# Kernel tuning notes

Hardware: AMD Instinct MI355X
Metric: run time of the kernel (lower is better)

## Reference

```python
import jax, jax.numpy as jnp
import numpy as np

B, L, H = 16, 4096, 256

def setup_inputs() -> dict:
    key = jax.random.key(0)
    k1, k2, k3 = jax.random.split(key, 3)
    scale = 1.0 / np.sqrt(H)
    x = jax.random.normal(k1, (B, L, H), dtype=jnp.float32)
    Wv = jax.random.normal(k2, (H, H), dtype=jnp.float32) * scale  # value_proj weight (torch Linear: y = x @ W.T)
    Wo = jax.random.normal(k3, (H, H), dtype=jnp.float32) * scale  # out_proj weight
    return {"x": x, "Wv": Wv, "Wo": Wo}

def reference(x, Wv, Wo):
    # x: [B, L, H]
    Bx, Lx, Hx = x.shape
    # Causal uniform-average 'attention' matrix: T[i, j] = 1/(i+1) for j <= i, else 0.
    tril = jnp.tril(jnp.ones((Lx, Lx), dtype=x.dtype))
    counts = jnp.arange(1, Lx + 1, dtype=x.dtype)[:, None]  # row-wise counts = i+1
    T = tril / counts
    # v = out_proj(value_proj(x)); torch Linear applies W.T on the right
    v = (x @ Wv.T) @ Wo.T                       # [B, L, H]
    # mixed[b, i] = mean over j <= i of v[b, j]  (== causal cumulative mean)
    mixed = jnp.einsum('ij,bjh->bih', T, v)     # [B, L, H]
    # dropout is identity in eval mode; pre_ln residual
    return x + mixed
```

## Files before the change

### kernel.cpp

```cpp
#include <hip/hip_runtime.h>
#include <hip/hip_bf16.h>


#define B_  16
#define L_  4096
#define H_  256
#define M_  (B_*L_)
#define CH  64
#define CHROWS 64
#define BM 64

typedef short short4v __attribute__((ext_vector_type(4)));
typedef short short8  __attribute__((ext_vector_type(8)));
typedef float f32x4   __attribute__((ext_vector_type(4)));

__device__ __forceinline__ unsigned short f2bf(float f) {
  unsigned int u = __builtin_bit_cast(unsigned int, f);
  u += 0x7fffu + ((u >> 16) & 1u);
  return (unsigned short)(u >> 16);
}
__device__ __forceinline__ float bf2f(unsigned short s) {
  return __builtin_bit_cast(float, ((unsigned int)s) << 16);
}

__global__ void fuse_w_kernel(const float* __restrict__ Wv,
                              const float* __restrict__ Wo,
                              unsigned short* __restrict__ Wbf) {
  __shared__ float wo[H_];
  int h = blockIdx.x, t = threadIdx.x;
  wo[t] = Wo[h*H_ + t];
  __syncthreads();
  float acc = 0.f;
  #pragma unroll 8
  for (int m = 0; m < H_; ++m) acc += wo[m] * Wv[m*H_ + t];
  Wbf[h*H_ + t] = f2bf(acc);
}

__global__ void partial_kernel(const float* __restrict__ x, float* __restrict__ P) {
  int c = blockIdx.x, b = blockIdx.y, t = threadIdx.x;
  const float* p = x + ((size_t)(b*L_ + c*CHROWS))*H_ + t;
  float s = 0.f;
  #pragma unroll 8
  for (int r = 0; r < CHROWS; ++r) s += p[(size_t)r*H_];
  P[(b*CH + c)*H_ + t] = s;
}

__global__ void scan_kernel(const float* __restrict__ P, float* __restrict__ O) {
  int b = blockIdx.x, t = threadIdx.x;
  float run = 0.f;
  #pragma unroll
  for (int c = 0; c < CH; ++c) {
    int idx = (b*CH + c)*H_ + t;
    O[idx] = run;
    run += P[idx];
  }
}

__global__ __launch_bounds__(512, 4) void main_kernel(
    const float* __restrict__ x,
    const unsigned short* __restrict__ Wbf,
    const float* __restrict__ Op,
    float* __restrict__ out) {
  __shared__ __align__(16) char smem[69632];
  float* zpart = (float*)(smem + 67584);

  const int tid = threadIdx.x;
  const int lane = tid & 63, wave = tid >> 6;
  const int rowBase = blockIdx.x * BM;

  float4 xk[8];
  const float* xb = x + (size_t)rowBase * H_;
  #pragma unroll
  for (int j = 0; j < 8; ++j)
    xk[j] = *(const float4*)(xb + (j*8 + wave)*H_ + lane*4);

  {
    const int c = tid & 255, h = tid >> 8;
    const float* op = Op + (size_t)blockIdx.x * H_ + h*128;
    const unsigned short* wr = Wbf + (size_t)c * H_ + h*128;
    float z = 0.f;
    #pragma unroll 4
    for (int kk = 0; kk < 16; ++kk) {
      short8 w8 = *(const short8*)(wr + kk*8);
      #pragma unroll
      for (int e = 0; e < 8; ++e) z += op[kk*8 + e] * bf2f((unsigned short)w8[e]);
    }
    zpart[h*256 + c] = z;
  }

  #pragma unroll
  for (int j = 0; j < 8; ++j) {
    int r = j*8 + wave;
    short4v s;
    s[0] = (short)f2bf(xk[j].x); s[1] = (short)f2bf(xk[j].y);
    s[2] = (short)f2bf(xk[j].z); s[3] = (short)f2bf(xk[j].w);
    *(short4v*)(smem + r*512 + ((lane*8) ^ ((r & 7) << 4))) = s;
  }
  __syncthreads();

  const int wc = wave;
  const int lrow = lane & 15, g = lane >> 4;
  f32x4 acc[4][2] = {};
  #pragma unroll
  for (int k0 = 0; k0 < 4; ++k0) {
    #pragma unroll
    for (int ks = 0; ks < 2; ++ks) {
      short8 bfr[2], af[4];
      #pragma unroll
      for (int n = 0; n < 2; ++n) {
        int wrow = wc*32 + n*16 + lrow;
        bfr[n] = *(const short8*)(Wbf + (size_t)wrow*H_ + k0*64 + ks*32 + g*8);
      }
      #pragma unroll
      for (int i = 0; i < 4; ++i) {
        int ar = i*16 + lrow;
        int cb = (k0*128 + ks*64 + g*16) ^ ((ar & 7) << 4);
        af[i] = *(const short8*)(smem + ar*512 + cb);
      }
      #pragma unroll
      for (int i = 0; i < 4; ++i)
        #pragma unroll
        for (int n = 0; n < 2; ++n)
          acc[i][n] = __builtin_amdgcn_mfma_f32_16x16x32_bf16(af[i], bfr[n], acc[i][n], 0, 0, 0);
    }
  }

  float base[2];
  #pragma unroll
  for (int n = 0; n < 2; ++n) {
    int c = wc*32 + n*16 + lrow;
    base[n] = zpart[c] + zpart[256 + c];
  }
  #pragma unroll
  for (int n = 0; n < 2; ++n) {
    float run = 0.f;
    #pragma unroll
    for (int i = 0; i < 4; ++i) {
      f32x4 a = acc[i][n];
      a[1] += a[0]; a[2] += a[1]; a[3] += a[2];
      float Bv = a[3];
      float v = Bv, t;
      t = __shfl_up(v, 16); if (lane >= 16) v += t;
      t = __shfl_up(v, 32); if (lane >= 32) v += t;
      float gex = v - Bv;
      float tot = __shfl(v, lrow + 48);
      float addv = gex + run + base[n];
      #pragma unroll
      for (int q = 0; q < 4; ++q) {
        int row = rowBase + i*16 + g*4 + q;
        float scale = 1.0f / (float)((row & (L_-1)) + 1);
        a[q] = (a[q] + addv) * scale;
      }
      acc[i][n] = a;
      run += tot;
    }
  }
  __syncthreads();

  #pragma unroll
  for (int i = 0; i < 4; ++i)
    #pragma unroll
    for (int n = 0; n < 2; ++n)
      #pragma unroll
      for (int q = 0; q < 4; ++q) {
        int row = i*16 + g*4 + q, col = wc*32 + n*16 + lrow;
        *(float*)(smem + row*1040 + col*4) = acc[i][n][q];
      }
  __syncthreads();

  float* ob = out + (size_t)rowBase * H_;
  #pragma unroll
  for (int j = 0; j < 8; ++j) {
    int r = j*8 + wave;
    f32x4 y = *(const f32x4*)(smem + r*1040 + lane*16);
    float4 o;
    o.x = xk[j].x + y[0]; o.y = xk[j].y + y[1];
    o.z = xk[j].z + y[2]; o.w = xk[j].w + y[3];
    *(float4*)(ob + r*H_ + lane*4) = o;
  }
}

extern "C" void kernel_launch(void* const* d_in, const int* in_sizes, int n_in,
                              void* d_out, int out_size, void* d_ws, size_t ws_size,
                              hipStream_t stream) {
  const float* x  = (const float*)d_in[0];
  const float* Wv = (const float*)d_in[1];
  const float* Wo = (const float*)d_in[2];
  float* out = (float*)d_out;

  char* ws = (char*)d_ws;
  unsigned short* Wbf = (unsigned short*)ws;
  float* P  = (float*)(ws + 131072);
  float* Op = (float*)(ws + 131072 + 1048576);

  hipLaunchKernelGGL(fuse_w_kernel,  dim3(H_),     dim3(H_), 0, stream, Wv, Wo, Wbf);
  hipLaunchKernelGGL(partial_kernel, dim3(CH, B_), dim3(H_), 0, stream, x, P);
  hipLaunchKernelGGL(scan_kernel,    dim3(B_),     dim3(H_), 0, stream, P, Op);
  hipLaunchKernelGGL(main_kernel,    dim3(M_/BM),  dim3(512), 0, stream,
                     x, Wbf, Op, out);
}
```

Before: 81.35 us.

## Halve main kernel block to 256 threads and stage output as bf16 in LDS

The main kernel now runs 4 waves per block instead of 8, and each wave computes 64 output columns (4x4 MFMA tiles) rather than 32. The carry-in vector z is computed by one thread per column without a split reduction. Output staging in shared memory switches from fp32 to swizzled bf16, shrinking LDS use so more blocks can be resident. Instead of keeping x in registers, the residual add re-reads it from global memory. The bf16 rounding of the mixed term adds precision loss, and the re-read adds global traffic.

```diff
diff --git a/kernel.cpp b/kernel.cpp
--- a/kernel.cpp
+++ b/kernel.cpp
@@ -56,59 +56,60 @@
   }
 }
 
-__global__ __launch_bounds__(512, 4) void main_kernel(
+__global__ __launch_bounds__(256, 4) void main_kernel(
     const float* __restrict__ x,
     const unsigned short* __restrict__ Wbf,
     const float* __restrict__ Op,
     float* __restrict__ out) {
-  __shared__ __align__(16) char smem[69632];
-  float* zpart = (float*)(smem + 67584);
+  __shared__ __align__(16) char smem[33792];
+  float* zbuf = (float*)(smem + 32768);
 
   const int tid = threadIdx.x;
   const int lane = tid & 63, wave = tid >> 6;
   const int rowBase = blockIdx.x * BM;
-
-  float4 xk[8];
   const float* xb = x + (size_t)rowBase * H_;
-  #pragma unroll
-  for (int j = 0; j < 8; ++j)
-    xk[j] = *(const float4*)(xb + (j*8 + wave)*H_ + lane*4);
+
+  float4 xv[16];
+  #pragma unroll
+  for (int j = 0; j < 16; ++j) {
+    int idx = tid + j*256;
+    xv[j] = *(const float4*)(xb + (idx >> 6)*H_ + (idx & 63)*4);
+  }
 
   {
-    const int c = tid & 255, h = tid >> 8;
-    const float* op = Op + (size_t)blockIdx.x * H_ + h*128;
-    const unsigned short* wr = Wbf + (size_t)c * H_ + h*128;
-    float z = 0.f;
-    #pragma unroll 4
-    for (int kk = 0; kk < 16; ++kk) {
+    const float* op = Op + (size_t)blockIdx.x * H_;
+    const unsigned short* wr = Wbf + (size_t)tid * H_;
+    float ze[8] = {0,0,0,0,0,0,0,0};
+    #pragma unroll
+    for (int kk = 0; kk < 32; ++kk) {
       short8 w8 = *(const short8*)(wr + kk*8);
       #pragma unroll
-      for (int e = 0; e < 8; ++e) z += op[kk*8 + e] * bf2f((unsigned short)w8[e]);
+      for (int e = 0; e < 8; ++e) ze[e] += op[kk*8 + e] * bf2f((unsigned short)w8[e]);
     }
-    zpart[h*256 + c] = z;
-  }
-
-  #pragma unroll
-  for (int j = 0; j < 8; ++j) {
-    int r = j*8 + wave;
+    zbuf[tid] = ((ze[0]+ze[1]) + (ze[2]+ze[3])) + ((ze[4]+ze[5]) + (ze[6]+ze[7]));
+  }
+
+  #pragma unroll
+  for (int j = 0; j < 16; ++j) {
+    int idx = tid + j*256;
+    int row = idx >> 6, col4 = idx & 63;
     short4v s;
-    s[0] = (short)f2bf(xk[j].x); s[1] = (short)f2bf(xk[j].y);
-    s[2] = (short)f2bf(xk[j].z); s[3] = (short)f2bf(xk[j].w);
-    *(short4v*)(smem + r*512 + ((lane*8) ^ ((r & 7) << 4))) = s;
-  }
-  __syncthreads();
-
-  const int wc = wave;
+    s[0] = (short)f2bf(xv[j].x); s[1] = (short)f2bf(xv[j].y);
+    s[2] = (short)f2bf(xv[j].z); s[3] = (short)f2bf(xv[j].w);
+    *(short4v*)(smem + row*512 + ((col4*8) ^ ((row & 7) << 4))) = s;
+  }
+  __syncthreads();
+
   const int lrow = lane & 15, g = lane >> 4;
-  f32x4 acc[4][2] = {};
+  f32x4 acc[4][4] = {};
   #pragma unroll
   for (int k0 = 0; k0 < 4; ++k0) {
     #pragma unroll
     for (int ks = 0; ks < 2; ++ks) {
-      short8 bfr[2], af[4];
-      #pragma unroll
-      for (int n = 0; n < 2; ++n) {
-        int wrow = wc*32 + n*16 + lrow;
+      short8 bfr[4], af[4];
+      #pragma unroll
+      for (int n = 0; n < 4; ++n) {
+        int wrow = wave*64 + n*16 + lrow;
         bfr[n] = *(const short8*)(Wbf + (size_t)wrow*H_ + k0*64 + ks*32 + g*8);
       }
       #pragma unroll
@@ -120,19 +121,14 @@
       #pragma unroll
       for (int i = 0; i < 4; ++i)
         #pragma unroll
-        for (int n = 0; n < 2; ++n)
+        for (int n = 0; n < 4; ++n)
           acc[i][n] = __builtin_amdgcn_mfma_f32_16x16x32_bf16(af[i], bfr[n], acc[i][n], 0, 0, 0);
     }
   }
 
-  float base[2];
-  #pragma unroll
-  for (int n = 0; n < 2; ++n) {
-    int c = wc*32 + n*16 + lrow;
-    base[n] = zpart[c] + zpart[256 + c];
-  }
-  #pragma unroll
-  for (int n = 0; n < 2; ++n) {
+  #pragma unroll
+  for (int n = 0; n < 4; ++n) {
+    float base = zbuf[wave*64 + n*16 + lrow];
     float run = 0.f;
     #pragma unroll
     for (int i = 0; i < 4; ++i) {
@@ -144,7 +140,7 @@
       t = __shfl_up(v, 32); if (lane >= 32) v += t;
       float gex = v - Bv;
       float tot = __shfl(v, lrow + 48);
-      float addv = gex + run + base[n];
+      float addv = gex + run + base;
       #pragma unroll
       for (int q = 0; q < 4; ++q) {
         int row = rowBase + i*16 + g*4 + q;
@@ -160,23 +156,29 @@
   #pragma unroll
   for (int i = 0; i < 4; ++i)
     #pragma unroll
-    for (int n = 0; n < 2; ++n)
+    for (int n = 0; n < 4; ++n)
       #pragma unroll
       for (int q = 0; q < 4; ++q) {
-        int row = i*16 + g*4 + q, col = wc*32 + n*16 + lrow;
-        *(float*)(smem + row*1040 + col*4) = acc[i][n][q];
+        int row = i*16 + g*4 + q;
+        int col = wave*64 + n*16 + lrow;
+        *(unsigned short*)(smem + row*512 + ((col*2) ^ ((row & 7) << 4))) =
+            f2bf(acc[i][n][q]);
       }
   __syncthreads();
 
   float* ob = out + (size_t)rowBase * H_;
   #pragma unroll
-  for (int j = 0; j < 8; ++j) {
-    int r = j*8 + wave;
-    f32x4 y = *(const f32x4*)(smem + r*1040 + lane*16);
+  for (int j = 0; j < 16; ++j) {
+    int idx = tid + j*256;
+    int row = idx >> 6, col4 = idx & 63;
+    short4v s = *(const short4v*)(smem + row*512 + ((col4*8) ^ ((row & 7) << 4)));
+    float4 xr = *(const float4*)(xb + row*H_ + col4*4);
     float4 o;
-    o.x = xk[j].x + y[0]; o.y = xk[j].y + y[1];
-    o.z = xk[j].z + y[2]; o.w = xk[j].w + y[3];
-    *(float4*)(ob + r*H_ + lane*4) = o;
+    o.x = xr.x + bf2f((unsigned short)s[0]);
+    o.y = xr.y + bf2f((unsigned short)s[1]);
+    o.z = xr.z + bf2f((unsigned short)s[2]);
+    o.w = xr.w + bf2f((unsigned short)s[3]);
+    *(float4*)(ob + row*H_ + col4*4) = o;
   }
 }
 
@@ -196,6 +198,6 @@
   hipLaunchKernelGGL(fuse_w_kernel,  dim3(H_),     dim3(H_), 0, stream, Wv, Wo, Wbf);
   hipLaunchKernelGGL(partial_kernel, dim3(CH, B_), dim3(H_), 0, stream, x, P);
   hipLaunchKernelGGL(scan_kernel,    dim3(B_),     dim3(H_), 0, stream, P, Op);
-  hipLaunchKernelGGL(main_kernel,    dim3(M_/BM),  dim3(512), 0, stream,
+  hipLaunchKernelGGL(main_kernel,    dim3(M_/BM),  dim3(256), 0, stream,
                      x, Wbf, Op, out);
 }
```

Measured after the change: 107.0 us. +31.6%, slower.

## Precompute chunk-prefix projection in separate kernel and parallelize chunk scan

Applied to the files above, without the earlier changes.

Moves the per-block projection of the chunk-prefix sum (Op @ W) out of the main kernel into a new zmat kernel that uses an fp32 transposed copy of the fused weight. The single-thread-per-column serial scan over 64 chunks is replaced by a wave-level shuffle scan spread over more blocks. The main kernel then reads a precomputed base vector instead of doing a 256-length dot product per column, and its launch bounds drop the occupancy hint. This adds one more kernel launch and extra workspace traffic in exchange for a shorter main kernel.

```diff
diff --git a/kernel.cpp b/kernel.cpp
--- a/kernel.cpp
+++ b/kernel.cpp
@@ -25,7 +25,8 @@
 
 __global__ void fuse_w_kernel(const float* __restrict__ Wv,
                               const float* __restrict__ Wo,
-                              unsigned short* __restrict__ Wbf) {
+                              unsigned short* __restrict__ Wbf,
+                              float* __restrict__ WbfTf) {
   __shared__ float wo[H_];
   int h = blockIdx.x, t = threadIdx.x;
   wo[t] = Wo[h*H_ + t];
@@ -34,6 +35,7 @@
   #pragma unroll 8
   for (int m = 0; m < H_; ++m) acc += wo[m] * Wv[m*H_ + t];
   Wbf[h*H_ + t] = f2bf(acc);
+  WbfTf[t*H_ + h] = acc;
 }
 
 __global__ void partial_kernel(const float* __restrict__ x, float* __restrict__ P) {
@@ -46,47 +48,61 @@
 }
 
 __global__ void scan_kernel(const float* __restrict__ P, float* __restrict__ O) {
-  int b = blockIdx.x, t = threadIdx.x;
-  float run = 0.f;
-  #pragma unroll
-  for (int c = 0; c < CH; ++c) {
-    int idx = (b*CH + c)*H_ + t;
-    O[idx] = run;
-    run += P[idx];
-  }
-}
-
-__global__ __launch_bounds__(512, 4) void main_kernel(
+  int cg = blockIdx.x, b = blockIdx.y;
+  int lane = threadIdx.x & 63, w = threadIdx.x >> 6;
+  int col = cg*4 + w;
+  int idx = (b*CH + lane)*H_ + col;
+  float val = P[idx];
+  float inc = val, t;
+  t = __shfl_up(inc, 1);  if (lane >= 1)  inc += t;
+  t = __shfl_up(inc, 2);  if (lane >= 2)  inc += t;
+  t = __shfl_up(inc, 4);  if (lane >= 4)  inc += t;
+  t = __shfl_up(inc, 8);  if (lane >= 8)  inc += t;
+  t = __shfl_up(inc, 16); if (lane >= 16) inc += t;
+  t = __shfl_up(inc, 32); if (lane >= 32) inc += t;
+  O[idx] = inc - val;
+}
+
+__global__ void zmat_kernel(const float* __restrict__ Op,
+                            const float* __restrict__ WbfTf,
+                            float* __restrict__ Z) {
+  const int lane = threadIdx.x & 63;
+  const int r = blockIdx.x*4 + (threadIdx.x >> 6);
+  const float* op = Op + (size_t)r * H_;
+  f32x4 a0 = {0,0,0,0}, a1 = {0,0,0,0};
+  #pragma unroll 8
+  for (int k = 0; k < H_; k += 2) {
+    float o0 = op[k], o1 = op[k+1];
+    f32x4 w0 = *(const f32x4*)(WbfTf + (size_t)k*H_ + lane*4);
+    f32x4 w1 = *(const f32x4*)(WbfTf + (size_t)(k+1)*H_ + lane*4);
+    a0 += o0 * w0;
+    a1 += o1 * w1;
+  }
+  *(f32x4*)(Z + (size_t)r*H_ + lane*4) = a0 + a1;
+}
+
+__global__ __launch_bounds__(512) void main_kernel(
     const float* __restrict__ x,
     const unsigned short* __restrict__ Wbf,
-    const float* __restrict__ Op,
+    const float* __restrict__ Z,
     float* __restrict__ out) {
-  __shared__ __align__(16) char smem[69632];
-  float* zpart = (float*)(smem + 67584);
+  __shared__ __align__(16) char smem[66560];
 
   const int tid = threadIdx.x;
   const int lane = tid & 63, wave = tid >> 6;
+  const int lrow = lane & 15, g = lane >> 4;
   const int rowBase = blockIdx.x * BM;
+  const float* xb = x + (size_t)rowBase * H_;
+
+  float base[2];
+  #pragma unroll
+  for (int n = 0; n < 2; ++n)
+    base[n] = Z[(size_t)blockIdx.x*H_ + wave*32 + n*16 + lrow];
 
   float4 xk[8];
-  const float* xb = x + (size_t)rowBase * H_;
   #pragma unroll
   for (int j = 0; j < 8; ++j)
     xk[j] = *(const float4*)(xb + (j*8 + wave)*H_ + lane*4);
-
-  {
-    const int c = tid & 255, h = tid >> 8;
-    const float* op = Op + (size_t)blockIdx.x * H_ + h*128;
-    const unsigned short* wr = Wbf + (size_t)c * H_ + h*128;
-    float z = 0.f;
-    #pragma unroll 4
-    for (int kk = 0; kk < 16; ++kk) {
-      short8 w8 = *(const short8*)(wr + kk*8);
-      #pragma unroll
-      for (int e = 0; e < 8; ++e) z += op[kk*8 + e] * bf2f((unsigned short)w8[e]);
-    }
-    zpart[h*256 + c] = z;
-  }
 
   #pragma unroll
   for (int j = 0; j < 8; ++j) {
@@ -98,8 +114,6 @@
   }
   __syncthreads();
 
-  const int wc = wave;
-  const int lrow = lane & 15, g = lane >> 4;
   f32x4 acc[4][2] = {};
   #pragma unroll
   for (int k0 = 0; k0 < 4; ++k0) {
@@ -108,7 +122,7 @@
       short8 bfr[2], af[4];
       #pragma unroll
       for (int n = 0; n < 2; ++n) {
-        int wrow = wc*32 + n*16 + lrow;
+        int wrow = wave*32 + n*16 + lrow;
         bfr[n] = *(const short8*)(Wbf + (size_t)wrow*H_ + k0*64 + ks*32 + g*8);
       }
       #pragma unroll
@@ -125,12 +139,6 @@
     }
   }
 
-  float base[2];
-  #pragma unroll
-  for (int n = 0; n < 2; ++n) {
-    int c = wc*32 + n*16 + lrow;
-    base[n] = zpart[c] + zpart[256 + c];
-  }
   #pragma unroll
   for (int n = 0; n < 2; ++n) {
     float run = 0.f;
@@ -163,7 +171,7 @@
     for (int n = 0; n < 2; ++n)
       #pragma unroll
       for (int q = 0; q < 4; ++q) {
-        int row = i*16 + g*4 + q, col = wc*32 + n*16 + lrow;
+        int row = i*16 + g*4 + q, col = wave*32 + n*16 + lrow;
         *(float*)(smem + row*1040 + col*4) = acc[i][n][q];
       }
   __syncthreads();
@@ -190,12 +198,14 @@
 
   char* ws = (char*)d_ws;
   unsigned short* Wbf = (unsigned short*)ws;
-  float* P  = (float*)(ws + 131072);
-  float* Op = (float*)(ws + 131072 + 1048576);
-
-  hipLaunchKernelGGL(fuse_w_kernel,  dim3(H_),     dim3(H_), 0, stream, Wv, Wo, Wbf);
-  hipLaunchKernelGGL(partial_kernel, dim3(CH, B_), dim3(H_), 0, stream, x, P);
-  hipLaunchKernelGGL(scan_kernel,    dim3(B_),     dim3(H_), 0, stream, P, Op);
-  hipLaunchKernelGGL(main_kernel,    dim3(M_/BM),  dim3(512), 0, stream,
-                     x, Wbf, Op, out);
-}
+  float* WbfTf = (float*)(ws + 131072);
+  float* P  = (float*)(ws + 131072 + 262144);
+  float* Op = (float*)(ws + 131072 + 262144 + 1048576);
+  float* Z  = (float*)(ws + 131072 + 262144 + 2097152);
+
+  hipLaunchKernelGGL(fuse_w_kernel,  dim3(H_),     dim3(H_),  0, stream, Wv, Wo, Wbf, WbfTf);
+  hipLaunchKernelGGL(partial_kernel, dim3(CH, B_), dim3(H_),  0, stream, x, P);
+  hipLaunchKernelGGL(scan_kernel,    dim3(64, B_), dim3(256), 0, stream, P, Op);
+  hipLaunchKernelGGL(zmat_kernel,    dim3(256),    dim3(256), 0, stream, Op, WbfTf, Z);
+  hipLaunchKernelGGL(main_kernel,    dim3(M_/BM),  dim3(512), 0, stream, x, Wbf, Z, out);
+}
```

After: 100.2 us. 23.2% more time.
